# Kernel tuning notes

Hardware: AMD Instinct MI355X
Metric: run time of the kernel (lower is better)

## Reference

```python
import jax, jax.numpy as jnp
import numpy as np

H = 4
N = 50000
D_IN = 128
D_MODEL = 256
NCLASS = 40
B_S = 1
BH = B_S * H
LN_EPS = 1e-5


def sparse_perm_1D(indices, values, feats, n, bh):
    """Batched sparse (bh,n,n) @ dense (bh,n,d): gather -> scale -> segment-sum scatter."""
    gathered = feats[indices[0], indices[2]]              # (nnz, d)
    contrib = values[:, None] * gathered                   # (nnz, d)
    seg = indices[0] * n + indices[1]                      # (nnz,)
    out = jax.ops.segment_sum(contrib, seg, num_segments=bh * n)
    return out.reshape(bh, n, -1)


def layer_norm(x, gamma, beta):
    mu = jnp.mean(x, axis=-1, keepdims=True)
    var = jnp.var(x, axis=-1, keepdims=True)
    return (x - mu) * jax.lax.rsqrt(var + LN_EPS) * gamma + beta


def setup_inputs() -> dict:
    key = jax.random.key(0)
    k1, k2, k3, k4, k5, k6, k7 = jax.random.split(key, 7)
    # per-(batch*head) permutation sigma: nonzero at (b, i, sigma_b(i))
    perm_keys = jax.random.split(k1, BH)
    sigma = jax.vmap(lambda k: jax.random.permutation(k, N))(perm_keys)  # (BH, N)
    b_idx = jnp.repeat(jnp.arange(BH), N)
    row_idx = jnp.tile(jnp.arange(N), BH)
    col_idx = sigma.reshape(-1)
    perm_indices = jnp.stack([b_idx, row_idx, col_idx], axis=0).astype(jnp.int32)  # (3, BH*N)
    perm_values = jax.random.uniform(k2, (BH * N,), dtype=jnp.float32)
    features = jax.random.normal(k3, (B_S, N, D_IN), dtype=jnp.float32)
    appd = jax.random.normal(k4, (B_S, N, D_IN), dtype=jnp.float32)
    # parameters
    w_scale_in = 1.0 / np.sqrt(2 * D_IN)
    W_in = jax.random.uniform(k5, (2 * D_IN, D_MODEL), dtype=jnp.float32, minval=-w_scale_in, maxval=w_scale_in)
    b_in = jnp.zeros((D_MODEL,), dtype=jnp.float32)
    ln_gamma = jnp.ones((D_MODEL * H,), dtype=jnp.float32)
    ln_beta = jnp.zeros((D_MODEL * H,), dtype=jnp.float32)
    w_scale_h = 1.0 / np.sqrt(D_MODEL * H)
    W_head = jax.random.uniform(k6, (D_MODEL * H, NCLASS), dtype=jnp.float32, minval=-w_scale_h, maxval=w_scale_h)
    b_head = jax.random.uniform(k7, (NCLASS,), dtype=jnp.float32, minval=-w_scale_h, maxval=w_scale_h)
    return {"perm_indices": perm_indices, "perm_values": perm_values,
            "features": features, "appd": appd,
            "W_in": W_in, "b_in": b_in,
            "ln_gamma": ln_gamma, "ln_beta": ln_beta,
            "W_head": W_head, "b_head": b_head}


def reference(perm_indices, perm_values, features, appd, W_in, b_in, ln_gamma, ln_beta, W_head, b_head):
    # concat auxiliary features, replicate per head: (B_S,N,2*D_IN) -> (BH,N,2*D_IN)
    feat = jnp.concatenate([features, appd], axis=-1)
    feat = jnp.broadcast_to(feat[:, None], (B_S, H, N, 2 * D_IN)).reshape(BH, N, 2 * D_IN)
    # permute rows: perm @ feat
    x = sparse_perm_1D(perm_indices, perm_values, feat, N, BH)
    # ff_in + relu (dropout is identity at eval)
    x = jax.nn.relu(x @ W_in + b_in)                       # (BH, N, D_MODEL)
    # nlayers == nblocks == 0: compress/uncompress loops are empty
    # inverse permutation: perm^T @ x (swap row/col indices)
    idx_t = jnp.stack([perm_indices[0], perm_indices[2], perm_indices[1]], axis=0)
    y = sparse_perm_1D(idx_t, perm_values, x, N, BH)       # (BH, N, D_MODEL)
    # (B_S,H,N,D) -> (B_S,N,H*D)
    y = y.reshape(B_S, H, N, D_MODEL).transpose(0, 2, 1, 3).reshape(B_S, N, H * D_MODEL)
    y = layer_norm(y, ln_gamma, ln_beta)
    return y @ W_head + b_head                             # (B_S, N, NCLASS)
```

## Files before the change

### kernel.cpp

```cpp
#include <hip/hip_runtime.h>
#include <hip/hip_bf16.h>

#define NROW 50000
#define DIN 128
#define DM 256
#define HH 4
#define NC 40
#define BHN 200000
#define NBLK 782

typedef float f32x4 __attribute__((ext_vector_type(4)));
typedef short bf16x8 __attribute__((ext_vector_type(8)));

__device__ __forceinline__ unsigned short f2bf(float x) {
    unsigned int u = __float_as_uint(x);
    u += 0x7fffu + ((u >> 16) & 1u);
    return (unsigned short)(u >> 16);
}

__device__ __forceinline__ unsigned int pk2(float lo, float hi) {
    __hip_bfloat162 h = __float22bfloat162_rn(make_float2(lo, hi));
    return *(unsigned int*)&h;
}

__device__ __forceinline__ float bf2f(unsigned short s) {
    return __uint_as_float(((unsigned int)s) << 16);
}

__device__ __forceinline__ void gl_lds16(const unsigned short* g, unsigned short* l) {
    __builtin_amdgcn_global_load_lds(
        (const __attribute__((address_space(1))) unsigned int*)(g),
        (__attribute__((address_space(3))) unsigned int*)(l),
        16, 0, 0);
}

__global__ __launch_bounds__(256) void k_prep(const int* __restrict__ pi,
                                              const float* __restrict__ pv,
                                              const float* __restrict__ Win,
                                              const float* __restrict__ Wh,
                                              const float* __restrict__ gamma,
                                              const float* __restrict__ beta,
                                              const float* __restrict__ bh,
                                              float* __restrict__ vcol,
                                              unsigned short* __restrict__ Wpk,
                                              unsigned short* __restrict__ Wgpk,
                                              float* __restrict__ bias2) {
    const int bid = blockIdx.x, tid = threadIdx.x;
    if (bid < 782) {
        int k = bid * 256 + tid;
        if (k < BHN) {
            int b = (k >= 150000) ? 3 : (k >= 100000) ? 2 : (k >= 50000) ? 1 : 0;
            int col = pi[2 * BHN + k];
            vcol[b * NROW + col] = pv[k];
        }
    } else if (bid < 798) {
        int base = (bid - 782) * 512;
        #pragma unroll
        for (int q = 0; q < 2; ++q) {
            int s = base + q * 256 + tid;
            int ln = s & 63;
            int t  = (s >> 6) & 15;
            int kc = s >> 10;
            int n  = t * 16 + (ln & 15);
            int kb = kc * 32 + ((ln >> 4) << 3);
            union { unsigned int ui[4]; uint4 v4; } u;
            #pragma unroll
            for (int jj = 0; jj < 4; ++jj)
                u.ui[jj] = pk2(Win[(kb + 2 * jj) * DM + n], Win[(kb + 2 * jj + 1) * DM + n]);
            *(uint4*)&Wpk[s * 8] = u.v4;
        }
    } else if (bid < 810) {
        int base = (bid - 798) * 512;
        #pragma unroll
        for (int q = 0; q < 2; ++q) {
            int s = base + q * 256 + tid;
            int ln = s & 63;
            int u6 = s >> 6;
            int t  = u6 % 3;
            int v6 = u6 / 3;
            int kc = v6 & 7;
            int h  = v6 >> 3;
            int c  = t * 16 + (ln & 15);
            int d0 = h * 256 + kc * 32 + ((ln >> 4) << 3);
            union { unsigned int ui[4]; uint4 v4; } u;
            if (c < NC) {
                #pragma unroll
                for (int jj = 0; jj < 4; ++jj)
                    u.ui[jj] = pk2(gamma[d0 + 2 * jj] * Wh[(d0 + 2 * jj) * NC + c],
                                   gamma[d0 + 2 * jj + 1] * Wh[(d0 + 2 * jj + 1) * NC + c]);
            } else {
                u.v4 = make_uint4(0u, 0u, 0u, 0u);
            }
            *(uint4*)&Wgpk[s * 8] = u.v4;
        }
    } else {
        __shared__ float red[256];
        int c = bid - 810;
        float sb = 0.f;
        #pragma unroll
        for (int q = 0; q < 4; ++q) {
            int d = tid + 256 * q;
            sb = fmaf(beta[d], Wh[d * NC + c], sb);
        }
        red[tid] = sb;
        __syncthreads();
        for (int st = 128; st > 0; st >>= 1) {
            if (tid < st) red[tid] += red[tid + st];
            __syncthreads();
        }
        if (tid == 0) bias2[c] = bh[c] + red[0];
    }
}

__global__ __launch_bounds__(256, 3) void k_fused(
    const float* __restrict__ feats, const float* __restrict__ appd,
    const unsigned short* __restrict__ Wpk,
    const unsigned short* __restrict__ Wgpk,
    const float* __restrict__ vcol,
    const float* __restrict__ b_in,
    const float* __restrict__ bias2,
    float* __restrict__ out)
{
    __shared__ __align__(16) unsigned short stage[8192];
    __shared__ __align__(16) unsigned short Gb[4][16 * 264];
    __shared__ float rsS[4][16], nmS[4][16];

    const int tid = threadIdx.x;
    const int wv = tid >> 6;
    const int ln = tid & 63;
    const int quad = ln >> 4;
    const int lr = ln & 15;
    const int j0 = blockIdx.x * 64;
    const int jw = j0 + wv * 16;
    const int ar = min(jw + lr, NROW - 1);

    const f32x4 zero4 = {0.f, 0.f, 0.f, 0.f};

    f32x4 accG[16];
    #pragma unroll
    for (int t = 0; t < 16; ++t) accG[t] = zero4;

    float4 x0 = *(const float4*)&feats[(size_t)ar * DIN + quad * 8];
    float4 x1 = *(const float4*)&feats[(size_t)ar * DIN + quad * 8 + 4];

    #pragma unroll 1
    for (int kc = 0; kc < 8; ++kc) {
        __syncthreads();
        #pragma unroll
        for (int q = 0; q < 4; ++q) {
            int f = wv * 4 + q;
            gl_lds16(Wpk + ((size_t)((kc * 16 + f) * 64 + ln)) * 8, &stage[f * 512]);
        }
        __syncthreads();

        union { unsigned int ui[4]; bf16x8 v; } a;
        a.ui[0] = pk2(x0.x, x0.y); a.ui[1] = pk2(x0.z, x0.w);
        a.ui[2] = pk2(x1.x, x1.y); a.ui[3] = pk2(x1.z, x1.w);
        if (kc < 7) {
            const float* srcn = (kc + 1 < 4) ? feats : appd;
            const int kon = ((kc + 1) & 3) * 32 + quad * 8;
            x0 = *(const float4*)&srcn[(size_t)ar * DIN + kon];
            x1 = *(const float4*)&srcn[(size_t)ar * DIN + kon + 4];
        }
        #pragma unroll
        for (int t = 0; t < 16; ++t) {
            bf16x8 bf = *(const bf16x8*)&stage[(t * 64 + ln) * 8];
            accG[t] = __builtin_amdgcn_mfma_f32_16x16x32_bf16(a.v, bf, accG[t], 0, 0, 0);
        }
    }

    float vhh[HH][4];
    #pragma unroll
    for (int h = 0; h < HH; ++h)
        #pragma unroll
        for (int rg = 0; rg < 4; ++rg)
            vhh[h][rg] = vcol[h * NROW + min(jw + quad * 4 + rg, NROW - 1)];

    float s_[4] = {0.f, 0.f, 0.f, 0.f}, ss_[4] = {0.f, 0.f, 0.f, 0.f};
    #pragma unroll
    for (int t = 0; t < 16; ++t) {
        float bt = b_in[t * 16 + lr];
        #pragma unroll
        for (int rg = 0; rg < 4; ++rg) {
            float gg = accG[t][rg];
            Gb[wv][(quad * 4 + rg) * 264 + t * 16 + lr] = f2bf(gg);
            #pragma unroll
            for (int h = 0; h < HH; ++h) {
                float v = vhh[h][rg];
                float y = v * fmaxf(fmaf(v, gg, bt), 0.f);
                s_[rg] += y;
                ss_[rg] = fmaf(y, y, ss_[rg]);
            }
        }
    }
    #pragma unroll
    for (int m = 1; m <= 8; m <<= 1)
        #pragma unroll
        for (int rg = 0; rg < 4; ++rg) {
            s_[rg] += __shfl_xor(s_[rg], m);
            ss_[rg] += __shfl_xor(ss_[rg], m);
        }
    if (lr == 0) {
        #pragma unroll
        for (int rg = 0; rg < 4; ++rg) {
            float mm = s_[rg] * (1.f / 1024.f);
            float var = ss_[rg] * (1.f / 1024.f) - mm * mm;
            float r_ = rsqrtf(var + 1e-5f);
            rsS[wv][quad * 4 + rg] = r_;
            nmS[wv][quad * 4 + rg] = -mm * r_;
        }
    }
    __syncthreads();

    float vm[HH];
    #pragma unroll
    for (int h = 0; h < HH; ++h) vm[h] = vcol[h * NROW + ar];
    const float rsm = rsS[wv][lr], nmm = nmS[wv][lr];

    f32x4 accO[3];
    #pragma unroll
    for (int t = 0; t < 3; ++t) accO[t] = zero4;

    #pragma unroll 1
    for (int ch = 0; ch < 8; ++ch) {
        const int h = ch >> 1;
        const int k0 = (ch & 1) * 4;
        #pragma unroll
        for (int q = 0; q < 3; ++q) {
            int s = wv * 3 + q;
            gl_lds16(Wgpk + ((size_t)((((h * 8 + k0 + wv) * 3 + q)) * 64 + ln)) * 8,
                     &stage[s * 512]);
        }
        __syncthreads();
        #pragma unroll
        for (int kcr = 0; kcr < 4; ++kcr) {
            const int kc = k0 + kcr;
            bf16x8 gf = *(const bf16x8*)&Gb[wv][lr * 264 + kc * 32 + quad * 8];
            float4 bA = *(const float4*)&b_in[kc * 32 + quad * 8];
            float4 bB = *(const float4*)&b_in[kc * 32 + quad * 8 + 4];
            float bb[8] = {bA.x, bA.y, bA.z, bA.w, bB.x, bB.y, bB.z, bB.w};
            union { unsigned int ui[4]; bf16x8 v; } u;
            #pragma unroll
            for (int jj = 0; jj < 4; ++jj) {
                float ya = vm[h] * fmaxf(fmaf(vm[h], bf2f((unsigned short)gf[2 * jj]), bb[2 * jj]), 0.f);
                float yb = vm[h] * fmaxf(fmaf(vm[h], bf2f((unsigned short)gf[2 * jj + 1]), bb[2 * jj + 1]), 0.f);
                u.ui[jj] = pk2(fmaf(ya, rsm, nmm), fmaf(yb, rsm, nmm));
            }
            #pragma unroll
            for (int t = 0; t < 3; ++t) {
                bf16x8 wf = *(const bf16x8*)&stage[((kcr * 3 + t) * 64 + ln) * 8];
                accO[t] = __builtin_amdgcn_mfma_f32_16x16x32_bf16(u.v, wf, accO[t], 0, 0, 0);
            }
        }
        __syncthreads();
    }

    #pragma unroll
    for (int t = 0; t < 3; ++t) {
        int c = t * 16 + lr;
        if (c < NC) {
            float b2 = bias2[c];
            #pragma unroll
            for (int rg = 0; rg < 4; ++rg) {
                int row = jw + quad * 4 + rg;
                if (row < NROW)
                    out[(size_t)row * NC + c] = accO[t][rg] + b2;
            }
        }
    }
}

extern "C" void kernel_launch(void* const* d_in, const int* in_sizes, int n_in,
                              void* d_out, int out_size, void* d_ws, size_t ws_size,
                              hipStream_t stream) {
    const int*   pi    = (const int*)d_in[0];
    const float* pv    = (const float*)d_in[1];
    const float* feats = (const float*)d_in[2];
    const float* appd  = (const float*)d_in[3];
    const float* Win   = (const float*)d_in[4];
    const float* b_in  = (const float*)d_in[5];
    const float* gamma = (const float*)d_in[6];
    const float* beta  = (const float*)d_in[7];
    const float* Wh    = (const float*)d_in[8];
    const float* bh    = (const float*)d_in[9];
    float* out = (float*)d_out;

    char* w = (char*)d_ws;
    float*          vcolW  = (float*)w;
    unsigned short* WpkW   = (unsigned short*)(w + 800000);
    unsigned short* WgpkW  = (unsigned short*)(w + 931072);
    float*          bias2W = (float*)(w + 1029376);

    k_prep<<<850, 256, 0, stream>>>(pi, pv, Win, Wh, gamma, beta, bh, vcolW, WpkW, WgpkW, bias2W);
    k_fused<<<NBLK, 256, 0, stream>>>(feats, appd, WpkW, WgpkW, vcolW, b_in, bias2W, out);
}
```

Before: 144.6 us.

## Fold layernorm into head epilogue and keep hidden activations in registers

```diff
diff --git a/kernel.cpp b/kernel.cpp
--- a/kernel.cpp
+++ b/kernel.cpp
@@ -12,19 +12,9 @@
 typedef float f32x4 __attribute__((ext_vector_type(4)));
 typedef short bf16x8 __attribute__((ext_vector_type(8)));
 
-__device__ __forceinline__ unsigned short f2bf(float x) {
-    unsigned int u = __float_as_uint(x);
-    u += 0x7fffu + ((u >> 16) & 1u);
-    return (unsigned short)(u >> 16);
-}
-
 __device__ __forceinline__ unsigned int pk2(float lo, float hi) {
     __hip_bfloat162 h = __float22bfloat162_rn(make_float2(lo, hi));
     return *(unsigned int*)&h;
-}
-
-__device__ __forceinline__ float bf2f(unsigned short s) {
-    return __uint_as_float(((unsigned int)s) << 16);
 }
 
 __device__ __forceinline__ void gl_lds16(const unsigned short* g, unsigned short* l) {
@@ -44,7 +34,8 @@
                                               float* __restrict__ vcol,
                                               unsigned short* __restrict__ Wpk,
                                               unsigned short* __restrict__ Wgpk,
-                                              float* __restrict__ bias2) {
+                                              float* __restrict__ bias2,
+                                              float* __restrict__ wsum) {
     const int bid = blockIdx.x, tid = threadIdx.x;
     if (bid < 782) {
         int k = bid * 256 + tid;
@@ -56,8 +47,8 @@
     } else if (bid < 798) {
         int base = (bid - 782) * 512;
         #pragma unroll
-        for (int q = 0; q < 2; ++q) {
-            int s = base + q * 256 + tid;
+        for (int qq = 0; qq < 2; ++qq) {
+            int s = base + qq * 256 + tid;
             int ln = s & 63;
             int t  = (s >> 6) & 15;
             int kc = s >> 10;
@@ -72,8 +63,8 @@
     } else if (bid < 810) {
         int base = (bid - 798) * 512;
         #pragma unroll
-        for (int q = 0; q < 2; ++q) {
-            int s = base + q * 256 + tid;
+        for (int qq = 0; qq < 2; ++qq) {
+            int s = base + qq * 256 + tid;
             int ln = s & 63;
             int u6 = s >> 6;
             int t  = u6 % 3;
@@ -81,49 +72,52 @@
             int kc = v6 & 7;
             int h  = v6 >> 3;
             int c  = t * 16 + (ln & 15);
-            int d0 = h * 256 + kc * 32 + ((ln >> 4) << 3);
+            int dbase = h * 256 + kc * 32 + ((ln >> 4) << 2);
             union { unsigned int ui[4]; uint4 v4; } u;
             if (c < NC) {
                 #pragma unroll
-                for (int jj = 0; jj < 4; ++jj)
-                    u.ui[jj] = pk2(gamma[d0 + 2 * jj] * Wh[(d0 + 2 * jj) * NC + c],
-                                   gamma[d0 + 2 * jj + 1] * Wh[(d0 + 2 * jj + 1) * NC + c]);
+                for (int jj = 0; jj < 4; ++jj) {
+                    int dA = dbase + ((jj >> 1) << 4) + ((jj & 1) << 1);
+                    u.ui[jj] = pk2(gamma[dA] * Wh[dA * NC + c],
+                                   gamma[dA + 1] * Wh[(dA + 1) * NC + c]);
+                }
             } else {
                 u.v4 = make_uint4(0u, 0u, 0u, 0u);
             }
             *(uint4*)&Wgpk[s * 8] = u.v4;
         }
     } else {
-        __shared__ float red[256];
+        __shared__ float redb[256], redw[256];
         int c = bid - 810;
-        float sb = 0.f;
+        float sb = 0.f, sw = 0.f;
         #pragma unroll
         for (int q = 0; q < 4; ++q) {
             int d = tid + 256 * q;
-            sb = fmaf(beta[d], Wh[d * NC + c], sb);
-        }
-        red[tid] = sb;
+            float w = Wh[d * NC + c];
+            sb = fmaf(beta[d], w, sb);
+            sw = fmaf(gamma[d], w, sw);
+        }
+        redb[tid] = sb; redw[tid] = sw;
         __syncthreads();
         for (int st = 128; st > 0; st >>= 1) {
-            if (tid < st) red[tid] += red[tid + st];
+            if (tid < st) { redb[tid] += redb[tid + st]; redw[tid] += redw[tid + st]; }
             __syncthreads();
         }
-        if (tid == 0) bias2[c] = bh[c] + red[0];
-    }
-}
-
-__global__ __launch_bounds__(256, 3) void k_fused(
+        if (tid == 0) { bias2[c] = bh[c] + redb[0]; wsum[c] = redw[0]; }
+    }
+}
+
+__global__ __launch_bounds__(256, 4) void k_fused(
     const float* __restrict__ feats, const float* __restrict__ appd,
     const unsigned short* __restrict__ Wpk,
     const unsigned short* __restrict__ Wgpk,
     const float* __restrict__ vcol,
     const float* __restrict__ b_in,
     const float* __restrict__ bias2,
+    const float* __restrict__ wsum,
     float* __restrict__ out)
 {
-    __shared__ __align__(16) unsigned short stage[8192];
-    __shared__ __align__(16) unsigned short Gb[4][16 * 264];
-    __shared__ float rsS[4][16], nmS[4][16];
+    __shared__ __align__(16) unsigned short stage[16384];
 
     const int tid = threadIdx.x;
     const int wv = tid >> 6;
@@ -134,137 +128,145 @@
     const int jw = j0 + wv * 16;
     const int ar = min(jw + lr, NROW - 1);
 
+    unsigned int afr[8][4];
+    {
+        const float* rf = feats + (size_t)ar * DIN;
+        const float* ra = appd  + (size_t)ar * DIN;
+        #pragma unroll
+        for (int kc = 0; kc < 8; ++kc) {
+            const float* src = (kc < 4) ? rf : ra;
+            const int ko = (kc & 3) * 32 + quad * 8;
+            float4 x0 = *(const float4*)(src + ko);
+            float4 x1 = *(const float4*)(src + ko + 4);
+            afr[kc][0] = pk2(x0.x, x0.y);
+            afr[kc][1] = pk2(x0.z, x0.w);
+            afr[kc][2] = pk2(x1.x, x1.y);
+            afr[kc][3] = pk2(x1.z, x1.w);
+        }
+    }
+    float vm[HH];
+    #pragma unroll
+    for (int h = 0; h < HH; ++h) vm[h] = vcol[h * NROW + ar];
+
     const f32x4 zero4 = {0.f, 0.f, 0.f, 0.f};
-
     f32x4 accG[16];
     #pragma unroll
     for (int t = 0; t < 16; ++t) accG[t] = zero4;
 
-    float4 x0 = *(const float4*)&feats[(size_t)ar * DIN + quad * 8];
-    float4 x1 = *(const float4*)&feats[(size_t)ar * DIN + quad * 8 + 4];
-
     #pragma unroll 1
-    for (int kc = 0; kc < 8; ++kc) {
-        __syncthreads();
-        #pragma unroll
-        for (int q = 0; q < 4; ++q) {
-            int f = wv * 4 + q;
-            gl_lds16(Wpk + ((size_t)((kc * 16 + f) * 64 + ln)) * 8, &stage[f * 512]);
-        }
-        __syncthreads();
-
-        union { unsigned int ui[4]; bf16x8 v; } a;
-        a.ui[0] = pk2(x0.x, x0.y); a.ui[1] = pk2(x0.z, x0.w);
-        a.ui[2] = pk2(x1.x, x1.y); a.ui[3] = pk2(x1.z, x1.w);
-        if (kc < 7) {
-            const float* srcn = (kc + 1 < 4) ? feats : appd;
-            const int kon = ((kc + 1) & 3) * 32 + quad * 8;
-            x0 = *(const float4*)&srcn[(size_t)ar * DIN + kon];
-            x1 = *(const float4*)&srcn[(size_t)ar * DIN + kon + 4];
-        }
-        #pragma unroll
-        for (int t = 0; t < 16; ++t) {
-            bf16x8 bf = *(const bf16x8*)&stage[(t * 64 + ln) * 8];
-            accG[t] = __builtin_amdgcn_mfma_f32_16x16x32_bf16(a.v, bf, accG[t], 0, 0, 0);
-        }
-    }
-
-    float vhh[HH][4];
-    #pragma unroll
-    for (int h = 0; h < HH; ++h)
-        #pragma unroll
-        for (int rg = 0; rg < 4; ++rg)
-            vhh[h][rg] = vcol[h * NROW + min(jw + quad * 4 + rg, NROW - 1)];
-
-    float s_[4] = {0.f, 0.f, 0.f, 0.f}, ss_[4] = {0.f, 0.f, 0.f, 0.f};
-    #pragma unroll
-    for (int t = 0; t < 16; ++t) {
-        float bt = b_in[t * 16 + lr];
-        #pragma unroll
-        for (int rg = 0; rg < 4; ++rg) {
-            float gg = accG[t][rg];
-            Gb[wv][(quad * 4 + rg) * 264 + t * 16 + lr] = f2bf(gg);
-            #pragma unroll
-            for (int h = 0; h < HH; ++h) {
-                float v = vhh[h][rg];
-                float y = v * fmaxf(fmaf(v, gg, bt), 0.f);
-                s_[rg] += y;
-                ss_[rg] = fmaf(y, y, ss_[rg]);
-            }
-        }
-    }
-    #pragma unroll
-    for (int m = 1; m <= 8; m <<= 1)
-        #pragma unroll
-        for (int rg = 0; rg < 4; ++rg) {
-            s_[rg] += __shfl_xor(s_[rg], m);
-            ss_[rg] += __shfl_xor(ss_[rg], m);
-        }
-    if (lr == 0) {
-        #pragma unroll
-        for (int rg = 0; rg < 4; ++rg) {
-            float mm = s_[rg] * (1.f / 1024.f);
-            float var = ss_[rg] * (1.f / 1024.f) - mm * mm;
-            float r_ = rsqrtf(var + 1e-5f);
-            rsS[wv][quad * 4 + rg] = r_;
-            nmS[wv][quad * 4 + rg] = -mm * r_;
-        }
-    }
-    __syncthreads();
-
-    float vm[HH];
-    #pragma unroll
-    for (int h = 0; h < HH; ++h) vm[h] = vcol[h * NROW + ar];
-    const float rsm = rsS[wv][lr], nmm = nmS[wv][lr];
-
+    for (int cc = 0; cc < 4; ++cc) {
+        __syncthreads();
+        #pragma unroll
+        for (int q = 0; q < 8; ++q) {
+            int f = wv * 8 + q;
+            gl_lds16(Wpk + ((size_t)((cc * 32 + f) * 64 + ln)) * 8, &stage[f * 512]);
+        }
+        __syncthreads();
+        #pragma unroll
+        for (int kcl = 0; kcl < 2; ++kcl) {
+            union { unsigned int ui[4]; bf16x8 v; } a;
+            a.ui[0] = afr[cc * 2 + kcl][0];
+            a.ui[1] = afr[cc * 2 + kcl][1];
+            a.ui[2] = afr[cc * 2 + kcl][2];
+            a.ui[3] = afr[cc * 2 + kcl][3];
+            #pragma unroll
+            for (int t = 0; t < 16; ++t) {
+                bf16x8 wf = *(const bf16x8*)&stage[((kcl * 16 + t) * 64 + ln) * 8];
+                accG[t] = __builtin_amdgcn_mfma_f32_16x16x32_bf16(wf, a.v, accG[t], 0, 0, 0);
+            }
+        }
+    }
+
+    float s_ = 0.f, ss_ = 0.f;
     f32x4 accO[3];
     #pragma unroll
     for (int t = 0; t < 3; ++t) accO[t] = zero4;
 
     #pragma unroll 1
-    for (int ch = 0; ch < 8; ++ch) {
-        const int h = ch >> 1;
-        const int k0 = (ch & 1) * 4;
-        #pragma unroll
-        for (int q = 0; q < 3; ++q) {
-            int s = wv * 3 + q;
-            gl_lds16(Wgpk + ((size_t)((((h * 8 + k0 + wv) * 3 + q)) * 64 + ln)) * 8,
-                     &stage[s * 512]);
-        }
-        __syncthreads();
-        #pragma unroll
-        for (int kcr = 0; kcr < 4; ++kcr) {
-            const int kc = k0 + kcr;
-            bf16x8 gf = *(const bf16x8*)&Gb[wv][lr * 264 + kc * 32 + quad * 8];
-            float4 bA = *(const float4*)&b_in[kc * 32 + quad * 8];
-            float4 bB = *(const float4*)&b_in[kc * 32 + quad * 8 + 4];
-            float bb[8] = {bA.x, bA.y, bA.z, bA.w, bB.x, bB.y, bB.z, bB.w};
-            union { unsigned int ui[4]; bf16x8 v; } u;
-            #pragma unroll
-            for (int jj = 0; jj < 4; ++jj) {
-                float ya = vm[h] * fmaxf(fmaf(vm[h], bf2f((unsigned short)gf[2 * jj]), bb[2 * jj]), 0.f);
-                float yb = vm[h] * fmaxf(fmaf(vm[h], bf2f((unsigned short)gf[2 * jj + 1]), bb[2 * jj + 1]), 0.f);
-                u.ui[jj] = pk2(fmaf(ya, rsm, nmm), fmaf(yb, rsm, nmm));
-            }
-            #pragma unroll
-            for (int t = 0; t < 3; ++t) {
-                bf16x8 wf = *(const bf16x8*)&stage[((kcr * 3 + t) * 64 + ln) * 8];
-                accO[t] = __builtin_amdgcn_mfma_f32_16x16x32_bf16(u.v, wf, accO[t], 0, 0, 0);
-            }
-        }
-        __syncthreads();
-    }
-
+    for (int h = 0; h < HH; ++h) {
+        __syncthreads();
+        #pragma unroll
+        for (int q = 0; q < 6; ++q) {
+            int sl = wv * 6 + q;
+            gl_lds16(Wgpk + ((size_t)((h * 24 + sl) * 64 + ln)) * 8, &stage[sl * 512]);
+        }
+        const float vh = vm[h];
+        unsigned int ya[16];
+        #pragma unroll
+        for (int tt = 0; tt < 8; ++tt) {
+            float4 b4 = *(const float4*)&b_in[tt * 16 + quad * 4];
+            float y0 = vh * fmaxf(fmaf(vh, accG[tt][0], b4.x), 0.f);
+            float y1 = vh * fmaxf(fmaf(vh, accG[tt][1], b4.y), 0.f);
+            float y2 = vh * fmaxf(fmaf(vh, accG[tt][2], b4.z), 0.f);
+            float y3 = vh * fmaxf(fmaf(vh, accG[tt][3], b4.w), 0.f);
+            s_ += (y0 + y1) + (y2 + y3);
+            ss_ = fmaf(y0, y0, ss_); ss_ = fmaf(y1, y1, ss_);
+            ss_ = fmaf(y2, y2, ss_); ss_ = fmaf(y3, y3, ss_);
+            ya[tt * 2]     = pk2(y0, y1);
+            ya[tt * 2 + 1] = pk2(y2, y3);
+        }
+        __syncthreads();
+        #pragma unroll
+        for (int kcl = 0; kcl < 4; ++kcl) {
+            union { unsigned int ui[4]; bf16x8 v; } af;
+            af.ui[0] = ya[4 * kcl];     af.ui[1] = ya[4 * kcl + 1];
+            af.ui[2] = ya[4 * kcl + 2]; af.ui[3] = ya[4 * kcl + 3];
+            #pragma unroll
+            for (int t3 = 0; t3 < 3; ++t3) {
+                bf16x8 wf = *(const bf16x8*)&stage[((kcl * 3 + t3) * 64 + ln) * 8];
+                accO[t3] = __builtin_amdgcn_mfma_f32_16x16x32_bf16(af.v, wf, accO[t3], 0, 0, 0);
+            }
+        }
+        #pragma unroll
+        for (int tt = 8; tt < 16; ++tt) {
+            float4 b4 = *(const float4*)&b_in[tt * 16 + quad * 4];
+            float y0 = vh * fmaxf(fmaf(vh, accG[tt][0], b4.x), 0.f);
+            float y1 = vh * fmaxf(fmaf(vh, accG[tt][1], b4.y), 0.f);
+            float y2 = vh * fmaxf(fmaf(vh, accG[tt][2], b4.z), 0.f);
+            float y3 = vh * fmaxf(fmaf(vh, accG[tt][3], b4.w), 0.f);
+            s_ += (y0 + y1) + (y2 + y3);
+            ss_ = fmaf(y0, y0, ss_); ss_ = fmaf(y1, y1, ss_);
+            ss_ = fmaf(y2, y2, ss_); ss_ = fmaf(y3, y3, ss_);
+            ya[(tt - 8) * 2]     = pk2(y0, y1);
+            ya[(tt - 8) * 2 + 1] = pk2(y2, y3);
+        }
+        #pragma unroll
+        for (int kcl = 4; kcl < 8; ++kcl) {
+            union { unsigned int ui[4]; bf16x8 v; } af;
+            af.ui[0] = ya[4 * (kcl - 4)];     af.ui[1] = ya[4 * (kcl - 4) + 1];
+            af.ui[2] = ya[4 * (kcl - 4) + 2]; af.ui[3] = ya[4 * (kcl - 4) + 3];
+            #pragma unroll
+            for (int t3 = 0; t3 < 3; ++t3) {
+                bf16x8 wf = *(const bf16x8*)&stage[((kcl * 3 + t3) * 64 + ln) * 8];
+                accO[t3] = __builtin_amdgcn_mfma_f32_16x16x32_bf16(af.v, wf, accO[t3], 0, 0, 0);
+            }
+        }
+    }
+
+    s_  += __shfl_xor(s_, 16);  s_  += __shfl_xor(s_, 32);
+    ss_ += __shfl_xor(ss_, 16); ss_ += __shfl_xor(ss_, 32);
+    float mm  = s_ * (1.f / 1024.f);
+    float var = ss_ * (1.f / 1024.f) - mm * mm;
+    float rs  = rsqrtf(var + 1e-5f);
+    float nm  = -mm * rs;
+
+    float rs_r[4], nm_r[4];
+    #pragma unroll
+    for (int rg = 0; rg < 4; ++rg) {
+        int rloc = quad * 4 + rg;
+        rs_r[rg] = __shfl(rs, rloc);
+        nm_r[rg] = __shfl(nm, rloc);
+    }
     #pragma unroll
     for (int t = 0; t < 3; ++t) {
         int c = t * 16 + lr;
         if (c < NC) {
-            float b2 = bias2[c];
+            float w2 = wsum[c], b2 = bias2[c];
             #pragma unroll
             for (int rg = 0; rg < 4; ++rg) {
                 int row = jw + quad * 4 + rg;
                 if (row < NROW)
-                    out[(size_t)row * NC + c] = accO[t][rg] + b2;
+                    out[(size_t)row * NC + c] = fmaf(rs_r[rg], accO[t][rg], fmaf(nm_r[rg], w2, b2));
             }
         }
     }
@@ -290,7 +292,10 @@
     unsigned short* WpkW   = (unsigned short*)(w + 800000);
     unsigned short* WgpkW  = (unsigned short*)(w + 931072);
     float*          bias2W = (float*)(w + 1029376);
-
-    k_prep<<<850, 256, 0, stream>>>(pi, pv, Win, Wh, gamma, beta, bh, vcolW, WpkW, WgpkW, bias2W);
-    k_fused<<<NBLK, 256, 0, stream>>>(feats, appd, WpkW, WgpkW, vcolW, b_in, bias2W, out);
-}
+    float*          wsumW  = (float*)(w + 1029536);
+
+    k_prep<<<850, 256, 0, stream>>>(pi, pv, Win, Wh, gamma, beta, bh,
+                                    vcolW, WpkW, WgpkW, bias2W, wsumW);
+    k_fused<<<NBLK, 256, 0, stream>>>(feats, appd, WpkW, WgpkW, vcolW, b_in,
+                                      bias2W, wsumW, out);
+}
```

Measured after the change: 200.6 us. 38.7% more time.
